# Performance work log

Measured on AMD Instinct MI355X. Metric: run time of the kernel, lower is better.

## Reference

```python
import jax, jax.numpy as jnp
import numpy as np

C = 256
B, H, W = 2, 64, 64


def conv1x1(x, Wt, b):
    # x: [B, Cin, H, W], Wt: [Cout, Cin], b: [Cout]
    return jnp.einsum('bchw,oc->bohw', x, Wt) + b[None, :, None, None]


def setup_inputs() -> dict:
    key = jax.random.key(0)
    ks = jax.random.split(key, 16)
    s = 0.02
    d = {
        'input1': jax.random.normal(ks[0], (B, C, H, W), jnp.float32),
        'input2': jax.random.normal(ks[1], (B, C, H, W), jnp.float32),
        'Wq1': jax.random.normal(ks[2], (C // 4, C), jnp.float32) * s,
        'bq1': jnp.zeros((C // 4,), jnp.float32),
        'Wk1': jax.random.normal(ks[3], (C // 2, C), jnp.float32) * s,
        'bk1': jnp.zeros((C // 2,), jnp.float32),
        'Wv1': jax.random.normal(ks[4], (C, C), jnp.float32) * s,
        'bv1': jnp.zeros((C,), jnp.float32),
        'Wq2': jax.random.normal(ks[5], (C // 4, C), jnp.float32) * s,
        'bq2': jnp.zeros((C // 4,), jnp.float32),
        'Wk2': jax.random.normal(ks[6], (C // 2, C), jnp.float32) * s,
        'bk2': jnp.zeros((C // 2,), jnp.float32),
        'Wv2': jax.random.normal(ks[7], (C, C), jnp.float32) * s,
        'bv2': jnp.zeros((C,), jnp.float32),
        'gamma': jax.random.normal(ks[8], (1,), jnp.float32) * 0.1,
    }
    return d


def reference(input1, input2, Wq1, bq1, Wk1, bk1, Wv1, bv1,
              Wq2, bq2, Wk2, bk2, Wv2, bv2, gamma):
    b, c, h, w = input1.shape
    hw = h * w
    q1 = conv1x1(input1, Wq1, bq1)                      # [B, C/4, H, W]
    k1 = conv1x1(input1, Wk1, bk1).reshape(b, -1, hw)   # [B, C/2, HW]
    v1 = conv1x1(input1, Wv1, bv1).reshape(b, -1, hw)   # [B, C,   HW]
    q2 = conv1x1(input2, Wq2, bq2)
    k2 = conv1x1(input2, Wk2, bk2).reshape(b, -1, hw)
    v2 = conv1x1(input2, Wv2, bv2).reshape(b, -1, hw)

    # cat on new dim 2 then 'b c t h w -> b (c t) h w' interleaves q1/q2 channels
    q = jnp.stack([q1, q2], axis=2).reshape(b, c // 2, hw)  # [B, C/2, HW]
    q = q.transpose(0, 2, 1)                                # [B, HW, C/2]

    a1 = jax.nn.softmax(jnp.einsum('bnc,bcm->bnm', q, k1), axis=-1)  # [B, HW, HW]
    out1 = jnp.einsum('bcm,bnm->bcn', v1, a1).reshape(b, c, h, w)
    out1 = gamma[0] * out1 + input1

    a2 = jax.nn.softmax(jnp.einsum('bnc,bcm->bnm', q, k2), axis=-1)
    out2 = jnp.einsum('bcm,bnm->bcn', v2, a2).reshape(b, c, h, w)
    out2 = gamma[0] * out2 + input2
    return (out1, out2)
```

## Files before the change

### kernel.cpp

```cpp
#include <hip/hip_runtime.h>

typedef __attribute__((ext_vector_type(8)))  short bf16x8;
typedef __attribute__((ext_vector_type(4)))  float f32x4;
typedef __attribute__((ext_vector_type(16))) float f32x16;
typedef __attribute__((ext_vector_type(8)))  unsigned short u16x8;

#define HW 4096
#define CDIM 256

#if __has_builtin(__builtin_amdgcn_exp2f)
#define EXP2(x) __builtin_amdgcn_exp2f(x)
#else
#define EXP2(x) exp2f(x)
#endif

__device__ __forceinline__ unsigned short f2bf(float f) {
    union { float f; unsigned u; } v; v.f = f;
    unsigned r = v.u + 0x7fffu + ((v.u >> 16) & 1u);
    return (unsigned short)(r >> 16);
}
__device__ __forceinline__ float bf2f(unsigned short u) {
    union { unsigned u; float f; } v; v.u = ((unsigned)u) << 16;
    return v.f;
}
__device__ __forceinline__ unsigned pk2(float hi, float lo) {
    union { float f; unsigned u; } a, b; a.f = hi; b.f = lo;
    return __builtin_amdgcn_perm(a.u, b.u, 0x07060302u);
}
__device__ __forceinline__ void gl_lds16(const void* g, void* l) {
    __builtin_amdgcn_global_load_lds(
        (const __attribute__((address_space(1))) unsigned int*)(unsigned long long)g,
        (__attribute__((address_space(3))) unsigned int*)(unsigned int)(unsigned long long)l,
        16, 0, 0);
}

__global__ __launch_bounds__(256) void wpack_kernel(
    const float* __restrict__ Wq1, const float* __restrict__ Wk1,
    const float* __restrict__ Wv1, const float* __restrict__ Wq2,
    const float* __restrict__ Wk2, const float* __restrict__ Wv2,
    unsigned short* __restrict__ Wpk)
{
    const int i  = blockIdx.x * 256 + threadIdx.x;
    const int c4 = i & 63;
    const int r6 = i >> 6;
    const int inp = r6 / 448;
    const int o   = r6 - inp * 448;
    const float* src;
    int orow;
    if (o < 64)       { src = inp ? Wq2 : Wq1; orow = o; }
    else if (o < 192) { src = inp ? Wk2 : Wk1; orow = o - 64; }
    else              { src = inp ? Wv2 : Wv1; orow = o - 192; }
    const float4 v = *(const float4*)(src + (size_t)orow * CDIM + c4 * 4);
    uint2 pkd; pkd.x = pk2(v.y, v.x); pkd.y = pk2(v.w, v.z);
    ((uint2*)Wpk)[i] = pkd;
}

__global__ __launch_bounds__(256) void proj_kernel(
    const float* __restrict__ in1, const float* __restrict__ in2,
    const float* __restrict__ bq1, const float* __restrict__ bk1,
    const float* __restrict__ bv1, const float* __restrict__ bq2,
    const float* __restrict__ bk2, const float* __restrict__ bv2,
    const unsigned short* __restrict__ Wpk,
    unsigned short* __restrict__ Qg, unsigned short* __restrict__ Kg,
    unsigned short* __restrict__ Vg)
{
    __shared__ unsigned xb[32 * 128];

    const int bid   = blockIdx.x;
    const int ntile = bid & 127;
    const int inp   = (bid >> 7) & 1;
    const int b     = bid >> 8;

    const float* X  = (inp ? in2 : in1) + (size_t)b * CDIM * HW;
    const float* bq = inp ? bq2 : bq1;
    const float* bk = inp ? bk2 : bk1;
    const float* bv = inp ? bv2 : bv1;
    const unsigned short* Wb = Wpk + (size_t)inp * 448 * CDIM;

    const int tid  = threadIdx.x;
    const int lane = tid & 63;
    const int w    = tid >> 6;
    const int l15  = lane & 15, quad = lane >> 4;
    const int n0   = ntile * 32;

#pragma unroll
    for (int t = 0; t < 4; ++t) {
        const int idx = t * 256 + tid;
        const int cp  = idx >> 3;
        const int n4  = idx & 7;
        const float* p0 = X + (size_t)(cp * 2) * HW + n0 + n4 * 4;
        const float4 a = *(const float4*)p0;
        const float4 bb = *(const float4*)(p0 + HW);
        const float av[4] = {a.x, a.y, a.z, a.w};
        const float bv4[4] = {bb.x, bb.y, bb.z, bb.w};
#pragma unroll
        for (int r = 0; r < 4; ++r) {
            const int n = n4 * 4 + r;
            xb[n * 128 + (((cp >> 2) ^ (n & 7)) << 2) + (cp & 3)] = pk2(bv4[r], av[r]);
        }
    }
    __syncthreads();

    f32x4 acc[7][2];
#pragma unroll
    for (int i = 0; i < 7; ++i)
#pragma unroll
        for (int j = 0; j < 2; ++j) acc[i][j] = (f32x4){0.f, 0.f, 0.f, 0.f};

#pragma unroll
    for (int kk = 0; kk < 8; ++kk) {
        bf16x8 xf[2];
#pragma unroll
        for (int ns = 0; ns < 2; ++ns) {
            const int nrow = ns * 16 + l15;
            xf[ns] = *(const bf16x8*)&xb[nrow * 128 + (((kk * 4 + quad) ^ (nrow & 7)) << 2)];
        }
#pragma unroll
        for (int os = 0; os < 7; ++os) {
            const int ob = w * 7 + os;
            const int og = ob * 16 + l15;
            const bf16x8 wf = *(const bf16x8*)(Wb + (size_t)og * CDIM + kk * 32 + quad * 8);
            if (ob < 12) {
#pragma unroll
                for (int ns = 0; ns < 2; ++ns)
                    acc[os][ns] = __builtin_amdgcn_mfma_f32_16x16x32_bf16(xf[ns], wf, acc[os][ns], 0, 0, 0);
            } else {
#pragma unroll
                for (int ns = 0; ns < 2; ++ns)
                    acc[os][ns] = __builtin_amdgcn_mfma_f32_16x16x32_bf16(wf, xf[ns], acc[os][ns], 0, 0, 0);
            }
        }
    }

    const size_t qbase = (size_t)b * HW * 128;
    const size_t kbase = (size_t)(b * 2 + inp) * HW * 128;
    const size_t vbase = (size_t)(b * 2 + inp) * (size_t)CDIM * HW;
#pragma unroll
    for (int os = 0; os < 7; ++os) {
        const int ob = w * 7 + os;
        if (ob < 4) {
            const int o = ob * 16 + l15;
            const float bb = bq[o];
#pragma unroll
            for (int ns = 0; ns < 2; ++ns) {
                const f32x4 d = acc[os][ns];
#pragma unroll
                for (int r = 0; r < 4; ++r) {
                    const int n = n0 + ns * 16 + quad * 4 + r;
                    Qg[qbase + (size_t)n * 128 + 2 * o + inp] =
                        f2bf((d[r] + bb) * 1.4426950408889634f);
                }
            }
        } else if (ob < 12) {
            const int c = (ob - 4) * 16 + l15;
            const float bb = bk[c];
#pragma unroll
            for (int ns = 0; ns < 2; ++ns) {
                const f32x4 d = acc[os][ns];
#pragma unroll
                for (int r = 0; r < 4; ++r) {
                    const int n = n0 + ns * 16 + quad * 4 + r;
                    Kg[kbase + (size_t)n * 128 + c] = f2bf(d[r] + bb);
                }
            }
        } else {
            const int c0 = (ob - 12) * 16 + quad * 4;
#pragma unroll
            for (int ns = 0; ns < 2; ++ns) {
                const f32x4 d = acc[os][ns];
#pragma unroll
                for (int r = 0; r < 4; ++r) {
                    const int n = n0 + ns * 16 + l15;
                    Vg[vbase + (size_t)(c0 + r) * HW + n] = f2bf(d[r] + bv[c0 + r]);
                }
            }
        }
    }
}

__global__ __launch_bounds__(256, 2) void attn_kernel(
    const unsigned short* __restrict__ Qg, const unsigned short* __restrict__ Kg,
    const unsigned short* __restrict__ Vg,
    unsigned short* __restrict__ Op, float* __restrict__ Lp)
{
    __shared__ unsigned short kbuf[2][32 * 16 * 8];
    __shared__ unsigned short vbuf[2][256 * 4 * 8];

    const int bid = blockIdx.x;
    const int mq  = bid & 3;
    const int set = (bid >> 2) & 3;
    const int att = set & 1, b = set >> 1;
    const int nt  = bid >> 4;
    const int n0g = nt * 128;
    const int mbase = mq * 1024;
    const int tid = threadIdx.x;
    const int lane = tid & 63, w = tid >> 6;
    const int l31 = lane & 31, h = lane >> 5;

    const unsigned short* Qb = Qg + (size_t)b * HW * 128;
    const unsigned short* Kb = Kg + (size_t)(b * 2 + att) * HW * 128;
    const unsigned short* Vb = Vg + (size_t)(b * 2 + att) * (size_t)CDIM * HW;

    bf16x8 aQ[8];
    {
        const int n = n0g + w * 32 + l31;
#pragma unroll
        for (int kk = 0; kk < 8; ++kk)
            aQ[kk] = *(const bf16x8*)(Qb + (size_t)n * 128 + kk * 16 + h * 8);
    }

    f32x16 acc[8];
#pragma unroll
    for (int i = 0; i < 8; ++i)
#pragma unroll
        for (int r = 0; r < 16; ++r) acc[i][r] = 0.f;
    float lsum = 0.f;

    const unsigned short* ksrc[2]; unsigned short* kdst[2][2];
    const unsigned short* vsrc[4]; unsigned short* vdst[2][4];
#pragma unroll
    for (int t = 0; t < 2; ++t) {
        const int L = (t * 4 + w) * 64 + lane;
        const int ml = L >> 4, s = L & 15;
        const int g = s ^ (ml & 15);
        ksrc[t] = Kb + (size_t)ml * 128 + g * 8;
        kdst[0][t] = &kbuf[0][L * 8]; kdst[1][t] = &kbuf[1][L * 8];
    }
#pragma unroll
    for (int t = 0; t < 4; ++t) {
        const int L = (t * 4 + w) * 64 + lane;
        const int c = L >> 2, s = L & 3;
        const int g = s ^ ((c >> 2) & 3);
        vsrc[t] = Vb + (size_t)c * HW + g * 8;
        vdst[0][t] = &vbuf[0][L * 8]; vdst[1][t] = &vbuf[1][L * 8];
    }

    auto stage = [&](int mt, int bs) {
        const int m0 = mbase + mt * 32;
#pragma unroll
        for (int t = 0; t < 2; ++t) gl_lds16(ksrc[t] + (size_t)m0 * 128, kdst[bs][t]);
#pragma unroll
        for (int t = 0; t < 4; ++t) gl_lds16(vsrc[t] + m0, vdst[bs][t]);
    };

    stage(0, 0);

    for (int mt = 0; mt < 32; ++mt) {
        __syncthreads();
        if (mt + 1 < 32) stage(mt + 1, (mt + 1) & 1);
        const int cur = mt & 1;

        f32x16 sa, sb;
#pragma unroll
        for (int r = 0; r < 16; ++r) { sa[r] = 0.f; sb[r] = 0.f; }
#pragma unroll
        for (int kk = 0; kk < 4; ++kk) {
            bf16x8 bK = *(const bf16x8*)&kbuf[cur][(l31 * 16 + ((kk * 2 + h) ^ (l31 & 15))) * 8];
            sa = __builtin_amdgcn_mfma_f32_32x32x16_bf16(bK, aQ[kk], sa, 0, 0, 0);
        }
#pragma unroll
        for (int kk = 4; kk < 8; ++kk) {
            bf16x8 bK = *(const bf16x8*)&kbuf[cur][(l31 * 16 + ((kk * 2 + h) ^ (l31 & 15))) * 8];
            sb = __builtin_amdgcn_mfma_f32_32x32x16_bf16(bK, aQ[kk], sb, 0, 0, 0);
        }

        float p[16];
#pragma unroll
        for (int r = 0; r < 16; ++r) {
            p[r] = EXP2(sa[r] + sb[r]);
            lsum += p[r];
        }

        bf16x8 bP[2];
#pragma unroll
        for (int k2 = 0; k2 < 2; ++k2) {
            const float* pp = p + k2 * 8;
            const unsigned a0 = pk2(pp[1], pp[0]);
            const unsigned a1 = pk2(pp[3], pp[2]);
            const unsigned b0 = pk2(pp[5], pp[4]);
            const unsigned b1 = pk2(pp[7], pp[6]);
            auto s0 = __builtin_amdgcn_permlane32_swap(a0, b0, false, false);
            auto s1 = __builtin_amdgcn_permlane32_swap(a1, b1, false, false);
            union { unsigned u[4]; bf16x8 v; } uu;
            uu.u[0] = s0[0];
            uu.u[1] = s1[0];
            uu.u[2] = s0[1];
            uu.u[3] = s1[1];
            bP[k2] = uu.v;
        }

#pragma unroll
        for (int cf = 0; cf < 8; ++cf) {
            const int c = cf * 32 + l31;
#pragma unroll
            for (int k2 = 0; k2 < 2; ++k2) {
                bf16x8 aV = *(const bf16x8*)&vbuf[cur][(c * 4 + ((k2 * 2 + h) ^ ((c >> 2) & 3))) * 8];
                acc[cf] = __builtin_amdgcn_mfma_f32_32x32x16_bf16(aV, bP[k2], acc[cf], 0, 0, 0);
            }
        }
    }

    const float ltot = lsum + __shfl_xor(lsum, 32, 64);
    const int nn = n0g + w * 32 + l31;
    if (h == 0) Lp[(size_t)(mq * 4 + set) * HW + nn] = ltot;

    const size_t obase = (size_t)(mq * 4 + set) * CDIM * HW;
#pragma unroll
    for (int cf = 0; cf < 8; ++cf) {
#pragma unroll
        for (int r = 0; r < 16; ++r) {
            const int c = cf * 32 + (r & 3) + 8 * (r >> 2) + 4 * h;
            Op[obase + (size_t)c * HW + nn] = f2bf(acc[cf][r]);
        }
    }
}

__global__ __launch_bounds__(256) void combine_kernel(
    const unsigned short* __restrict__ Op, const float* __restrict__ Lp,
    const float* __restrict__ in1, const float* __restrict__ in2,
    const float* __restrict__ gamma_p, float* __restrict__ out)
{
    const size_t i8 = ((size_t)blockIdx.x * 256 + threadIdx.x) * 8;
    const int oset = (int)(i8 >> 20);
    const int att = oset >> 1, b = oset & 1;
    const int pset = b * 2 + att;
    const size_t rem = i8 & 1048575u;
    const int n = (int)(i8 & 4095);

    u16x8 o[4];
    f32x4 l0[4], l1[4];
#pragma unroll
    for (int mq = 0; mq < 4; ++mq) {
        o[mq]  = *(const u16x8*)(Op + ((size_t)(mq * 4 + pset) << 20) + rem);
        l0[mq] = *(const f32x4*)(Lp + (size_t)(mq * 4 + pset) * HW + n);
        l1[mq] = *(const f32x4*)(Lp + (size_t)(mq * 4 + pset) * HW + n + 4);
    }
    const float* inb = (att ? in2 : in1) + (size_t)b * CDIM * HW + rem;
    const float g = *gamma_p;

    const f32x4 iv0 = *(const f32x4*)(inb);
    const f32x4 iv1 = *(const f32x4*)(inb + 4);
    f32x4 r0, r1;
#pragma unroll
    for (int j = 0; j < 4; ++j) {
        float ov = 0.f, ld = 0.f;
#pragma unroll
        for (int mq = 0; mq < 4; ++mq) {
            ov += bf2f((unsigned short)o[mq][j]);
            ld += l0[mq][j];
        }
        r0[j] = g * ov / ld + iv0[j];
    }
#pragma unroll
    for (int j = 0; j < 4; ++j) {
        float ov = 0.f, ld = 0.f;
#pragma unroll
        for (int mq = 0; mq < 4; ++mq) {
            ov += bf2f((unsigned short)o[mq][j + 4]);
            ld += l1[mq][j];
        }
        r1[j] = g * ov / ld + iv1[j];
    }
    *(f32x4*)(out + i8) = r0;
    *(f32x4*)(out + i8 + 4) = r1;
}

extern "C" void kernel_launch(void* const* d_in, const int* in_sizes, int n_in,
                              void* d_out, int out_size, void* d_ws, size_t ws_size,
                              hipStream_t stream) {
    const float* in1 = (const float*)d_in[0];
    const float* in2 = (const float*)d_in[1];
    const float* Wq1 = (const float*)d_in[2];  const float* bq1 = (const float*)d_in[3];
    const float* Wk1 = (const float*)d_in[4];  const float* bk1 = (const float*)d_in[5];
    const float* Wv1 = (const float*)d_in[6];  const float* bv1 = (const float*)d_in[7];
    const float* Wq2 = (const float*)d_in[8];  const float* bq2 = (const float*)d_in[9];
    const float* Wk2 = (const float*)d_in[10]; const float* bk2 = (const float*)d_in[11];
    const float* Wv2 = (const float*)d_in[12]; const float* bv2 = (const float*)d_in[13];
    const float* gamma = (const float*)d_in[14];

    unsigned short* Qg = (unsigned short*)d_ws;
    unsigned short* Kg = Qg + (size_t)2 * HW * 128;
    unsigned short* Vg = Kg + (size_t)4 * HW * 128;
    unsigned short* Op = Vg + (size_t)4 * CDIM * HW;
    float*          Lp = (float*)(Op + (size_t)16 * CDIM * HW);
    unsigned short* Wpk = Op;

    wpack_kernel<<<224, 256, 0, stream>>>(Wq1, Wk1, Wv1, Wq2, Wk2, Wv2, Wpk);
    proj_kernel<<<512, 256, 0, stream>>>(in1, in2, bq1, bk1, bv1, bq2, bk2, bv2,
                                         Wpk, Qg, Kg, Vg);
    attn_kernel<<<512, 256, 0, stream>>>(Qg, Kg, Vg, Op, Lp);
    combine_kernel<<<2048, 256, 0, stream>>>(Op, Lp, in1, in2, gamma, (float*)d_out);
}
```

Before: 179.2 us.

## Software-pipeline attention loop: overlap next tile's QK/exp with current PV

Restructures the attention main loop so that the QK^T MFMAs and exp for tile i+1 are issued alongside the PV MFMAs for tile i, using two ping-pong P register sets. The V buffer becomes triple-buffered so the V tile of the previous step stays resident while the next one loads, and the loop is manually unrolled by two. Source/destination pointers are replaced by compact offsets to save registers. The aim is to hide exp/pack latency behind MFMA work, at the cost of more LDS and more live registers, which may lower occupancy.

New measurement: 493.9 us. 2.76x slower.

```diff
diff --git a/kernel.cpp b/kernel.cpp
--- a/kernel.cpp
+++ b/kernel.cpp
@@ -184,7 +184,7 @@
     unsigned short* __restrict__ Op, float* __restrict__ Lp)
 {
     __shared__ unsigned short kbuf[2][32 * 16 * 8];
-    __shared__ unsigned short vbuf[2][256 * 4 * 8];
+    __shared__ unsigned short vbuf[3][256 * 4 * 8];
 
     const int bid = blockIdx.x;
     const int mq  = bid & 3;
@@ -216,62 +216,56 @@
         for (int r = 0; r < 16; ++r) acc[i][r] = 0.f;
     float lsum = 0.f;
 
-    const unsigned short* ksrc[2]; unsigned short* kdst[2][2];
-    const unsigned short* vsrc[4]; unsigned short* vdst[2][4];
+    unsigned koff[2], voff[4];
 #pragma unroll
     for (int t = 0; t < 2; ++t) {
         const int L = (t * 4 + w) * 64 + lane;
         const int ml = L >> 4, s = L & 15;
-        const int g = s ^ (ml & 15);
-        ksrc[t] = Kb + (size_t)ml * 128 + g * 8;
-        kdst[0][t] = &kbuf[0][L * 8]; kdst[1][t] = &kbuf[1][L * 8];
+        koff[t] = (unsigned)(ml * 128 + (s ^ (ml & 15)) * 8);
     }
 #pragma unroll
     for (int t = 0; t < 4; ++t) {
         const int L = (t * 4 + w) * 64 + lane;
         const int c = L >> 2, s = L & 3;
-        const int g = s ^ ((c >> 2) & 3);
-        vsrc[t] = Vb + (size_t)c * HW + g * 8;
-        vdst[0][t] = &vbuf[0][L * 8]; vdst[1][t] = &vbuf[1][L * 8];
-    }
-
-    auto stage = [&](int mt, int bs) {
+        voff[t] = (unsigned)(c * HW + (s ^ ((c >> 2) & 3)) * 8);
+    }
+
+    auto stage = [&](int mt) {
+        const int kb = mt & 1;
+        const int vb = mt % 3;
         const int m0 = mbase + mt * 32;
 #pragma unroll
-        for (int t = 0; t < 2; ++t) gl_lds16(ksrc[t] + (size_t)m0 * 128, kdst[bs][t]);
-#pragma unroll
-        for (int t = 0; t < 4; ++t) gl_lds16(vsrc[t] + m0, vdst[bs][t]);
+        for (int t = 0; t < 2; ++t)
+            gl_lds16(Kb + (size_t)m0 * 128 + koff[t],
+                     (char*)(&kbuf[kb][0]) + (size_t)(t * 4 + w) * 1024);
+#pragma unroll
+        for (int t = 0; t < 4; ++t)
+            gl_lds16(Vb + (size_t)m0 + voff[t],
+                     (char*)(&vbuf[vb][0]) + (size_t)(t * 4 + w) * 1024);
     };
 
-    stage(0, 0);
-
-    for (int mt = 0; mt < 32; ++mt) {
-        __syncthreads();
-        if (mt + 1 < 32) stage(mt + 1, (mt + 1) & 1);
-        const int cur = mt & 1;
-
-        f32x16 sa, sb;
+    auto QK = [&](const unsigned short* kb_, f32x16& sa, f32x16& sb) {
 #pragma unroll
         for (int r = 0; r < 16; ++r) { sa[r] = 0.f; sb[r] = 0.f; }
 #pragma unroll
         for (int kk = 0; kk < 4; ++kk) {
-            bf16x8 bK = *(const bf16x8*)&kbuf[cur][(l31 * 16 + ((kk * 2 + h) ^ (l31 & 15))) * 8];
+            bf16x8 bK = *(const bf16x8*)&kb_[(l31 * 16 + ((kk * 2 + h) ^ (l31 & 15))) * 8];
             sa = __builtin_amdgcn_mfma_f32_32x32x16_bf16(bK, aQ[kk], sa, 0, 0, 0);
         }
 #pragma unroll
         for (int kk = 4; kk < 8; ++kk) {
-            bf16x8 bK = *(const bf16x8*)&kbuf[cur][(l31 * 16 + ((kk * 2 + h) ^ (l31 & 15))) * 8];
+            bf16x8 bK = *(const bf16x8*)&kb_[(l31 * 16 + ((kk * 2 + h) ^ (l31 & 15))) * 8];
             sb = __builtin_amdgcn_mfma_f32_32x32x16_bf16(bK, aQ[kk], sb, 0, 0, 0);
         }
-
+    };
+
+    auto EXPP = [&](const f32x16& sa, const f32x16& sb, bf16x8* bP) {
         float p[16];
 #pragma unroll
         for (int r = 0; r < 16; ++r) {
             p[r] = EXP2(sa[r] + sb[r]);
             lsum += p[r];
         }
-
-        bf16x8 bP[2];
 #pragma unroll
         for (int k2 = 0; k2 < 2; ++k2) {
             const float* pp = p + k2 * 8;
@@ -288,15 +282,48 @@
             uu.u[3] = s1[1];
             bP[k2] = uu.v;
         }
-
+    };
+
+    auto PV = [&](const unsigned short* vb_, const bf16x8* bP) {
 #pragma unroll
         for (int cf = 0; cf < 8; ++cf) {
             const int c = cf * 32 + l31;
 #pragma unroll
             for (int k2 = 0; k2 < 2; ++k2) {
-                bf16x8 aV = *(const bf16x8*)&vbuf[cur][(c * 4 + ((k2 * 2 + h) ^ ((c >> 2) & 3))) * 8];
+                bf16x8 aV = *(const bf16x8*)&vb_[(c * 4 + ((k2 * 2 + h) ^ ((c >> 2) & 3))) * 8];
                 acc[cf] = __builtin_amdgcn_mfma_f32_32x32x16_bf16(aV, bP[k2], acc[cf], 0, 0, 0);
             }
+        }
+    };
+
+    stage(0);
+    __syncthreads();
+    stage(1);
+    bf16x8 bPA[2], bPB[2];
+    {
+        f32x16 sa, sb;
+        QK(&kbuf[0][0], sa, sb);
+        EXPP(sa, sb, bPA);
+    }
+#pragma unroll 1
+    for (int i = 1; i <= 31; i += 2) {
+        __syncthreads();
+        if (i <= 30) stage(i + 1);
+        {
+            f32x16 sa, sb;
+            QK(&kbuf[1][0], sa, sb);
+            PV(&vbuf[(i - 1) % 3][0], bPA);
+            EXPP(sa, sb, bPB);
+        }
+        __syncthreads();
+        if (i <= 29) stage(i + 2);
+        if (i + 1 <= 31) {
+            f32x16 sa, sb;
+            QK(&kbuf[0][0], sa, sb);
+            PV(&vbuf[i % 3][0], bPB);
+            EXPP(sa, sb, bPA);
+        } else {
+            PV(&vbuf[i % 3][0], bPB);
         }
     }
 
```

## Triple-buffer K/V LDS staging with explicit vmcnt waits in attention loop

Applied to the files above, without the earlier changes.

Moves the attention kernel's K/V shared-memory staging from double to triple buffering, prefetching two tiles ahead. Each iteration waits with an explicit s_waitcnt vmcnt that lets the newest tile's loads stay in flight, and uses a raw s_barrier in place of __syncthreads. The aim is to hide global-to-LDS load latency behind MFMA work. In exchange LDS use rises by half, which may reduce occupancy at 2 blocks per CU, and the hand-written wait counts depend on the compiler emitting exactly the expected loads.

After: 179.2 us. Within noise of the previous version (+0.0%).

```diff
diff --git a/kernel.cpp b/kernel.cpp
--- a/kernel.cpp
+++ b/kernel.cpp
@@ -183,8 +183,8 @@
     const unsigned short* __restrict__ Vg,
     unsigned short* __restrict__ Op, float* __restrict__ Lp)
 {
-    __shared__ unsigned short kbuf[2][32 * 16 * 8];
-    __shared__ unsigned short vbuf[2][256 * 4 * 8];
+    __shared__ unsigned short kbuf[3][32 * 16 * 8];
+    __shared__ unsigned short vbuf[3][256 * 4 * 8];
 
     const int bid = blockIdx.x;
     const int mq  = bid & 3;
@@ -216,39 +216,44 @@
         for (int r = 0; r < 16; ++r) acc[i][r] = 0.f;
     float lsum = 0.f;
 
-    const unsigned short* ksrc[2]; unsigned short* kdst[2][2];
-    const unsigned short* vsrc[4]; unsigned short* vdst[2][4];
+    const unsigned short* ksrc[2];
+    const unsigned short* vsrc[4];
 #pragma unroll
     for (int t = 0; t < 2; ++t) {
         const int L = (t * 4 + w) * 64 + lane;
         const int ml = L >> 4, s = L & 15;
-        const int g = s ^ (ml & 15);
-        ksrc[t] = Kb + (size_t)ml * 128 + g * 8;
-        kdst[0][t] = &kbuf[0][L * 8]; kdst[1][t] = &kbuf[1][L * 8];
+        ksrc[t] = Kb + (size_t)ml * 128 + (s ^ (ml & 15)) * 8;
     }
 #pragma unroll
     for (int t = 0; t < 4; ++t) {
         const int L = (t * 4 + w) * 64 + lane;
         const int c = L >> 2, s = L & 3;
-        const int g = s ^ ((c >> 2) & 3);
-        vsrc[t] = Vb + (size_t)c * HW + g * 8;
-        vdst[0][t] = &vbuf[0][L * 8]; vdst[1][t] = &vbuf[1][L * 8];
+        vsrc[t] = Vb + (size_t)c * HW + (s ^ ((c >> 2) & 3)) * 8;
     }
 
     auto stage = [&](int mt, int bs) {
         const int m0 = mbase + mt * 32;
-#pragma unroll
-        for (int t = 0; t < 2; ++t) gl_lds16(ksrc[t] + (size_t)m0 * 128, kdst[bs][t]);
-#pragma unroll
-        for (int t = 0; t < 4; ++t) gl_lds16(vsrc[t] + m0, vdst[bs][t]);
+        char* kdl = (char*)&kbuf[bs][0] + (size_t)w * 1024;
+        char* vdl = (char*)&vbuf[bs][0] + (size_t)w * 1024;
+#pragma unroll
+        for (int t = 0; t < 2; ++t)
+            gl_lds16(ksrc[t] + (size_t)m0 * 128, kdl + (size_t)t * 4096);
+#pragma unroll
+        for (int t = 0; t < 4; ++t)
+            gl_lds16(vsrc[t] + m0, vdl + (size_t)t * 4096);
     };
 
     stage(0, 0);
-
+    stage(1, 1);
+
+    int cur = 0;
+    int nxt = 2;
+#pragma unroll 1
     for (int mt = 0; mt < 32; ++mt) {
-        __syncthreads();
-        if (mt + 1 < 32) stage(mt + 1, (mt + 1) & 1);
-        const int cur = mt & 1;
+        if (mt < 31) asm volatile("s_waitcnt vmcnt(6)" ::: "memory");
+        else         asm volatile("s_waitcnt vmcnt(0)" ::: "memory");
+        __builtin_amdgcn_s_barrier();
+        if (mt + 2 < 32) stage(mt + 2, nxt);
 
         f32x16 sa, sb;
 #pragma unroll
@@ -289,15 +294,19 @@
             bP[k2] = uu.v;
         }
 
+        const unsigned short* vb_ = &vbuf[cur][0];
 #pragma unroll
         for (int cf = 0; cf < 8; ++cf) {
             const int c = cf * 32 + l31;
 #pragma unroll
             for (int k2 = 0; k2 < 2; ++k2) {
-                bf16x8 aV = *(const bf16x8*)&vbuf[cur][(c * 4 + ((k2 * 2 + h) ^ ((c >> 2) & 3))) * 8];
+                bf16x8 aV = *(const bf16x8*)&vb_[(c * 4 + ((k2 * 2 + h) ^ ((c >> 2) & 3))) * 8];
                 acc[cf] = __builtin_amdgcn_mfma_f32_32x32x16_bf16(aV, bP[k2], acc[cf], 0, 0, 0);
             }
         }
+
+        cur = (cur == 2) ? 0 : cur + 1;
+        nxt = (nxt == 2) ? 0 : nxt + 1;
     }
 
     const float ltot = lsum + __shfl_xor(lsum, 32, 64);
```
